# Performance work log

Hardware: AMD Instinct MI355X
Metric: run time of the kernel (lower is better)

## Reference

```python
import jax, jax.numpy as jnp
import numpy as np
import math

DENOM = 32.0

# e3nn scalar_activation normalizes the activation to unit second moment under N(0,1).
# Compute the gelu normalization constant by Gauss-Hermite quadrature.
_zs, _ws = np.polynomial.hermite_e.hermegauss(64)
_g = 0.5 * _zs * (1.0 + np.array([math.erf(z / math.sqrt(2.0)) for z in _zs]))
C_GELU = float(1.0 / math.sqrt((_ws * _g * _g).sum() / math.sqrt(2.0 * math.pi)))


def _spherical_harmonics(r):
    # r: [E,3] unit vectors. Component-normalized real SH for l=1,2,3.
    x, y, z = r[..., 0], r[..., 1], r[..., 2]
    s3, s5, s15 = math.sqrt(3.0), math.sqrt(5.0), math.sqrt(15.0)
    s7, s105 = math.sqrt(7.0), math.sqrt(105.0)
    s35_8, s21_8 = math.sqrt(35.0 / 8.0), math.sqrt(21.0 / 8.0)
    Y1 = s3 * r                                                     # [E,3]
    Y2 = jnp.stack([s15 * x * y, s15 * y * z, 0.5 * s5 * (3 * z * z - 1),
                    s15 * x * z, 0.5 * s15 * (x * x - y * y)], -1)   # [E,5]
    Y3 = jnp.stack([s35_8 * y * (3 * x * x - y * y), s105 * x * y * z,
                    s21_8 * y * (5 * z * z - 1), 0.5 * s7 * z * (5 * z * z - 3),
                    s21_8 * x * (5 * z * z - 1), 0.5 * s105 * z * (x * x - y * y),
                    s35_8 * x * (x * x - 3 * y * y)], -1)            # [E,7]
    return [Y1, Y2, Y3]


def setup_inputs() -> dict:
    key = jax.random.key(0)
    k = jax.random.split(key, 7)
    N, E, MUL, TMUL = 32768, 1048576, 16, 32
    return {
        "x": jax.random.normal(k[0], (N, MUL), jnp.float32),
        "positions": jax.random.normal(k[1], (N, 3), jnp.float32),
        "W_pre": jax.random.normal(k[2], (4, MUL, TMUL), jnp.float32),
        "W_post": jax.random.normal(k[3], (4, TMUL, TMUL), jnp.float32),
        "W_shortcut": jax.random.normal(k[4], (MUL, TMUL), jnp.float32),
        "senders": jax.random.randint(k[5], (E,), 0, N, jnp.int32),
        "receivers": jax.random.randint(k[6], (E,), 0, N, jnp.int32),
    }


def reference(x, positions, W_pre, W_post, W_shortcut, senders, receivers):
    N, mul = x.shape
    tmul = W_pre.shape[-1]
    # --- edge update: sh of relative positions, tensor product with sender scalars ---
    rvec = positions[receivers] - positions[senders]                 # [E,3]
    n = jnp.linalg.norm(rvec, axis=-1, keepdims=True)
    rhat = rvec / jnp.where(n == 0, 1.0, n)
    Ys = _spherical_harmonics(rhat)
    s = x[senders]                                                   # [E,mul] (0e)
    # --- aggregate edge features at receivers (segment sum) ---
    agg = [jax.ops.segment_sum(s, receivers, num_segments=N)]        # 0e block
    for Y in Ys:
        e = (s[:, :, None] * Y[:, None, :]).reshape(s.shape[0], -1)  # 0e x l -> l
        agg.append(jax.ops.segment_sum(e, receivers, num_segments=N).reshape(N, mul, Y.shape[-1]))
    # --- node update: linear_pre -> scalar act -> linear_post, plus shortcut ---
    inv_in = 1.0 / math.sqrt(mul)
    inv_mid = 1.0 / math.sqrt(tmul)
    out = []
    for l in range(4):
        a = agg[l] / DENOM
        if l == 0:
            p = (a @ W_pre[0]) * inv_in
            p = C_GELU * jax.nn.gelu(p, approximate=False)           # act on 0e scalars only
            q = (p @ W_post[0]) * inv_mid
            q = q + (x @ W_shortcut) * inv_in                        # shortcut: only 0e path exists
            out.append(q)
        else:
            p = jnp.einsum('nui,uv->nvi', a, W_pre[l]) * inv_in
            q = jnp.einsum('nvi,vw->nwi', p, W_post[l]) * inv_mid
            out.append(q.reshape(N, -1))
    return jnp.concatenate(out, axis=-1)                              # [N, tmul*16]
```

## Files before the change

kernel.cpp:

```cpp
#include <hip/hip_runtime.h>
#include <math.h>

#define NN 32768
#define EN 1048576
#define NBIN 256
#define BINCAP 8192
#define TILE 4096

#define C_GELU_F 1.5335262f

__global__ __launch_bounds__(512) void bin_k(const int* __restrict__ snd,
                                             const int* __restrict__ rcv,
                                             const float* __restrict__ pos,
                                             float4* __restrict__ posw,
                                             int* __restrict__ bin_cur,
                                             unsigned* __restrict__ binbuf) {
    __shared__ unsigned cnt[NBIN];
    __shared__ unsigned excl[NBIN];
    __shared__ unsigned cur2[NBIN];
    __shared__ unsigned gbase[NBIN];
    __shared__ unsigned stage[TILE];
    int t = threadIdx.x;
    int tile = blockIdx.x * TILE;
    if (t < NBIN) { cnt[t] = 0; cur2[t] = 0; }
    if (t < 128) {
        int n = (blockIdx.x << 7) + t;
        posw[n] = make_float4(pos[3*n], pos[3*n+1], pos[3*n+2], 0.f);
    }
    __syncthreads();

    unsigned w[TILE / 512];
#pragma unroll
    for (int i = 0; i < TILE / 512; ++i) {
        int e = tile + i * 512 + t;
        unsigned r = (unsigned)rcv[e], s = (unsigned)snd[e];
        w[i] = (r << 15) | s;
        atomicAdd(&cnt[w[i] >> 22], 1u);
    }
    __syncthreads();

    unsigned my = (t < NBIN) ? cnt[t] : 0u;
    if (t < NBIN) excl[t] = my;
    __syncthreads();
    for (int d = 1; d < NBIN; d <<= 1) {
        unsigned v = (t < NBIN && t >= d) ? excl[t - d] : 0u;
        __syncthreads();
        if (t < NBIN) excl[t] += v;
        __syncthreads();
    }
    if (t < NBIN) {
        unsigned myexcl = excl[t] - my;
        gbase[t] = atomicAdd((unsigned*)&bin_cur[t], my);
        excl[t] = myexcl;
    }
    __syncthreads();

#pragma unroll
    for (int i = 0; i < TILE / 512; ++i) {
        unsigned b = w[i] >> 22;
        unsigned p = excl[b] + atomicAdd(&cur2[b], 1u);
        stage[p] = w[i];
    }
    __syncthreads();

    for (int p = t; p < TILE; p += 512) {
        unsigned ww = stage[p];
        unsigned b = ww >> 22;
        unsigned idx = gbase[b] + ((unsigned)p - excl[b]);
        if (idx < BINCAP) binbuf[b * BINCAP + idx] = ww;
    }
}

__global__ __launch_bounds__(1024) void csr_k(const int* __restrict__ bin_cur,
                                              const unsigned* __restrict__ binbuf,
                                              int* __restrict__ row_ptr,
                                              int* __restrict__ edge_csr) {
    __shared__ unsigned sc[NBIN];
    __shared__ unsigned cnt[128];
    __shared__ unsigned excl[128];
    __shared__ unsigned cur2[128];
    int b = blockIdx.x;
    int t = threadIdx.x;

    if (t < NBIN) sc[t] = (unsigned)bin_cur[t];
    __syncthreads();
    for (int d = 1; d < NBIN; d <<= 1) {
        unsigned v = (t < NBIN && t >= d) ? sc[t - d] : 0u;
        __syncthreads();
        if (t < NBIN) sc[t] += v;
        __syncthreads();
    }
    int Mraw = bin_cur[b];
    int base = (int)(sc[b] - (unsigned)Mraw);
    int M = Mraw > BINCAP ? BINCAP : Mraw;
    if (t < 128) { cnt[t] = 0; cur2[t] = 0; }
    __syncthreads();

    const unsigned* bb = binbuf + b * BINCAP;
    for (int i = t; i < M; i += 1024)
        atomicAdd(&cnt[(bb[i] >> 15) & 127], 1u);
    __syncthreads();

    if (t < 128) excl[t] = cnt[t];
    __syncthreads();
    for (int d = 1; d < 128; d <<= 1) {
        unsigned v = (t >= d && t < 128) ? excl[t - d] : 0u;
        __syncthreads();
        if (t < 128) excl[t] += v;
        __syncthreads();
    }
    if (t < 128) {
        unsigned e = excl[t] - cnt[t];
        excl[t] = e;
        row_ptr[(b << 7) + t] = base + (int)e;
        if (b == NBIN - 1 && t == 127) row_ptr[NN] = base + (int)(e + cnt[127]);
    }
    __syncthreads();

    for (int i = t; i < M; i += 1024) {
        unsigned ww = bb[i];
        unsigned r7 = (ww >> 15) & 127;
        unsigned dst = excl[r7] + atomicAdd(&cur2[r7], 1u);
        edge_csr[base + dst] = (int)(ww & 0x7FFF);
    }
}

#define GROUPS 32
#define BLK 512
#define YST 20
#define GST (16*YST + 8)

__global__ __launch_bounds__(512, 4) void fused_k(const float* __restrict__ x,
                                                  const float4* __restrict__ posw,
                                                  const int* __restrict__ row_ptr,
                                                  const int* __restrict__ edge_csr,
                                                  const float* __restrict__ Wpre,
                                                  const float* __restrict__ Wpost,
                                                  const float* __restrict__ Wsc,
                                                  float* __restrict__ out) {
    __shared__ float sPre[4*516];
    __shared__ float sPost[4*1028];
    __shared__ float sSc[512];
    __shared__ float sY[GROUPS * GST];

    int t = threadIdx.x;
    for (int idx = t; idx < 2048; idx += BLK)
        sPre[(idx >> 9)*516 + (idx & 511)] = Wpre[idx];
    for (int idx = t; idx < 4096; idx += BLK)
        sPost[(idx >> 10)*1028 + (idx & 1023)] = Wpost[idx];
    sSc[t] = Wsc[t];
    __syncthreads();

    int g = t >> 4;
    int j = t & 15;
    int n = blockIdx.x * GROUPS + g;
    int beg = row_ptr[n], end = row_ptr[n + 1];
    int cnt = end - beg;
    float4 rp = posw[n];
    float* yg = sY + g * GST;

    const float s3   = 1.7320508075688772f;
    const float s5   = 2.2360679774997896f;
    const float s15  = 3.8729833462074170f;
    const float s7   = 2.6457513110645907f;
    const float s105 = 10.246950765959598f;
    const float s35_8 = 2.0916500663351889f;
    const float s21_8 = 1.6201851746019651f;

    float acc[16];
#pragma unroll
    for (int u = 0; u < 16; ++u) acc[u] = 0.f;

    int nch = (cnt + 15) >> 4;
    if (nch > 0) {
        int ki0 = (j < cnt) ? j : cnt - 1;
        int sE = edge_csr[beg + ki0];
        float4 sp = posw[sE];

        for (int c = 0; c < nch; ++c) {
            int kn = ((c + 1) << 4) + j;
            int kiN = (kn < cnt) ? kn : cnt - 1;
            int sEn = edge_csr[beg + kiN];

            float vx = rp.x - sp.x, vy = rp.y - sp.y, vz = rp.z - sp.z;
            float n2 = vx*vx + vy*vy + vz*vz;
            float inv;
            if (n2 > 0.f) {
                inv = rsqrtf(n2);
                inv = inv * (1.5f - 0.5f * n2 * inv * inv);
            } else inv = 0.f;
            float X = vx*inv, Y = vy*inv, Z = vz*inv;
            float XX = X*X, YY = Y*Y, ZZ = Z*Z;
            float m = (((c << 4) + j) < cnt) ? 1.f : 0.f;

            float* yr = yg + j * YST;
            ((float4*)yr)[0] = make_float4(m, m*(s3*X), m*(s3*Y), m*(s3*Z));
            ((float4*)yr)[1] = make_float4(m*(s15*X*Y), m*(s15*Y*Z),
                                           m*(0.5f*s5*(3.f*ZZ - 1.f)), m*(s15*X*Z));
            ((float4*)yr)[2] = make_float4(m*(0.5f*s15*(XX - YY)),
                                           m*(s35_8*Y*(3.f*XX - YY)),
                                           m*(s105*X*Y*Z),
                                           m*(s21_8*Y*(5.f*ZZ - 1.f)));
            ((float4*)yr)[3] = make_float4(m*(0.5f*s7*Z*(5.f*ZZ - 3.f)),
                                           m*(s21_8*X*(5.f*ZZ - 1.f)),
                                           m*(0.5f*s105*Z*(XX - YY)),
                                           m*(s35_8*X*(XX - 3.f*YY)));

            int se[16];
#pragma unroll
            for (int e = 0; e < 16; ++e)
                se[e] = __shfl(sE, (t & 48) + e, 64);
            float yt[16];
#pragma unroll
            for (int e = 0; e < 16; ++e)
                yt[e] = yg[e * YST + j];

            float4 spn = posw[sEn];

#pragma unroll
            for (int e = 0; e < 16; ++e) {
                float y = yt[e];
                const float4* xp = (const float4*)(x + (se[e] << 4));
                float4 a0 = xp[0], a1 = xp[1], a2 = xp[2], a3 = xp[3];
                acc[0]  += a0.x * y;  acc[1]  += a0.y * y;
                acc[2]  += a0.z * y;  acc[3]  += a0.w * y;
                acc[4]  += a1.x * y;  acc[5]  += a1.y * y;
                acc[6]  += a1.z * y;  acc[7]  += a1.w * y;
                acc[8]  += a2.x * y;  acc[9]  += a2.y * y;
                acc[10] += a2.z * y;  acc[11] += a2.w * y;
                acc[12] += a3.x * y;  acc[13] += a3.y * y;
                acc[14] += a3.z * y;  acc[15] += a3.w * y;
            }

            sE = sEn; sp = spn;
        }
    }

    int l, i, offl, deg;
    if (j == 0)      { l = 0; i = 0;     offl = 0;   deg = 1; }
    else if (j < 4)  { l = 1; i = j - 1; offl = 32;  deg = 3; }
    else if (j < 9)  { l = 2; i = j - 4; offl = 128; deg = 5; }
    else             { l = 3; i = j - 9; offl = 288; deg = 7; }

    const float c1 = 0.0078125f;
    const float c2 = 0.17677669529663687f;

    float p[32];
#pragma unroll
    for (int v = 0; v < 32; ++v) p[v] = 0.f;
    const float* wp = sPre + l * 516;
#pragma unroll
    for (int uu = 0; uu < 16; ++uu) {
        float a = acc[uu];
        const float4* w4 = (const float4*)(wp + (uu << 5));
#pragma unroll
        for (int vq = 0; vq < 8; ++vq) {
            float4 w = w4[vq];
            p[4*vq+0] += a * w.x;
            p[4*vq+1] += a * w.y;
            p[4*vq+2] += a * w.z;
            p[4*vq+3] += a * w.w;
        }
    }
#pragma unroll
    for (int v = 0; v < 32; ++v) p[v] *= c1;

    if (j == 0) {
#pragma unroll
        for (int v = 0; v < 32; ++v) {
            float pv = p[v];
            p[v] = C_GELU_F * 0.5f * pv * (1.f + erff(pv * 0.7071067811865476f));
        }
    }

    float q[32];
#pragma unroll
    for (int w = 0; w < 32; ++w) q[w] = 0.f;
    const float* wq = sPost + l * 1028;
#pragma unroll
    for (int v = 0; v < 32; ++v) {
        float pv = p[v];
        const float4* w4 = (const float4*)(wq + (v << 5));
#pragma unroll
        for (int wd = 0; wd < 8; ++wd) {
            float4 w = w4[wd];
            q[4*wd+0] += pv * w.x;
            q[4*wd+1] += pv * w.y;
            q[4*wd+2] += pv * w.z;
            q[4*wd+3] += pv * w.w;
        }
    }
#pragma unroll
    for (int w = 0; w < 32; ++w) q[w] *= c2;

    if (j == 0) {
        const float* xp = x + (n << 4);
#pragma unroll
        for (int uu = 0; uu < 16; ++uu) {
            float xv = 0.25f * xp[uu];
            const float4* w4 = (const float4*)(sSc + (uu << 5));
#pragma unroll
            for (int wd = 0; wd < 8; ++wd) {
                float4 w = w4[wd];
                q[4*wd+0] += xv * w.x;
                q[4*wd+1] += xv * w.y;
                q[4*wd+2] += xv * w.z;
                q[4*wd+3] += xv * w.w;
            }
        }
    }

    float* op = out + (n << 9) + offl + i;
#pragma unroll
    for (int w = 0; w < 32; ++w) op[w * deg] = q[w];
}

extern "C" void kernel_launch(void* const* d_in, const int* in_sizes, int n_in,
                              void* d_out, int out_size, void* d_ws, size_t ws_size,
                              hipStream_t stream) {
    const float* x     = (const float*)d_in[0];
    const float* pos   = (const float*)d_in[1];
    const float* Wpre  = (const float*)d_in[2];
    const float* Wpost = (const float*)d_in[3];
    const float* Wsc   = (const float*)d_in[4];
    const int*   snd   = (const int*)d_in[5];
    const int*   rcv   = (const int*)d_in[6];
    float* out = (float*)d_out;

    char* ws = (char*)d_ws;
    int*      bin_cur   = (int*)(ws);
    int*      row_ptr   = (int*)(ws + 2048);
    float4*   posw      = (float4*)(ws + 0x30000);
    int*      edge_csr  = (int*)(ws + 0xB0000);
    unsigned* binbuf    = (unsigned*)(ws + 0x500000);

    hipMemsetAsync(bin_cur, 0, NBIN * sizeof(int), stream);
    bin_k<<<EN / TILE, 512, 0, stream>>>(snd, rcv, pos, posw, bin_cur, binbuf);
    csr_k<<<NBIN, 1024, 0, stream>>>(bin_cur, binbuf, row_ptr, edge_csr);
    fused_k<<<NN / GROUPS, BLK, 0, stream>>>(x, posw, row_ptr, edge_csr,
                                             Wpre, Wpost, Wsc, out);
}
```

Before: 186.1 us.

## Fold per-bin CSR construction into the fused node kernel, dropping csr_k

Raises the bin count to 1024 so each bin holds exactly the 32 receiver nodes that one fused_k block handles. Each fused_k block now loads its bin from binbuf, counting-sorts the edges by receiver in shared memory (16-bit sender ids, wave-level scan), and uses the resulting offsets directly. This removes the separate csr_k launch and the global row_ptr/edge_csr round trip. In exchange, bin_k scatters each tile into four times as many bins with fewer entries per bin, which makes its global writes less coalesced, and every fused block pays for a shared-memory sort before its main loop.

```diff
diff --git a/kernel.cpp b/kernel.cpp
--- a/kernel.cpp
+++ b/kernel.cpp
@@ -3,9 +3,9 @@
 
 #define NN 32768
 #define EN 1048576
-#define NBIN 256
-#define BINCAP 8192
-#define TILE 4096
+#define NBIN 1024
+#define BINCAP 2048
+#define TILE 2048
 
 #define C_GELU_F 1.5335262f
 
@@ -22,9 +22,9 @@
     __shared__ unsigned stage[TILE];
     int t = threadIdx.x;
     int tile = blockIdx.x * TILE;
-    if (t < NBIN) { cnt[t] = 0; cur2[t] = 0; }
-    if (t < 128) {
-        int n = (blockIdx.x << 7) + t;
+    cnt[t] = 0; cnt[t + 512] = 0; cur2[t] = 0; cur2[t + 512] = 0;
+    if (t < 64) {
+        int n = (blockIdx.x << 6) + t;
         posw[n] = make_float4(pos[3*n], pos[3*n+1], pos[3*n+2], 0.f);
     }
     __syncthreads();
@@ -35,29 +35,28 @@
         int e = tile + i * 512 + t;
         unsigned r = (unsigned)rcv[e], s = (unsigned)snd[e];
         w[i] = (r << 15) | s;
-        atomicAdd(&cnt[w[i] >> 22], 1u);
-    }
-    __syncthreads();
-
-    unsigned my = (t < NBIN) ? cnt[t] : 0u;
-    if (t < NBIN) excl[t] = my;
+        atomicAdd(&cnt[w[i] >> 20], 1u);
+    }
+    __syncthreads();
+
+    unsigned my0 = cnt[t], my1 = cnt[t + 512];
+    excl[t] = my0; excl[t + 512] = my1;
     __syncthreads();
     for (int d = 1; d < NBIN; d <<= 1) {
-        unsigned v = (t < NBIN && t >= d) ? excl[t - d] : 0u;
+        unsigned v0 = (t >= d) ? excl[t - d] : 0u;
+        unsigned v1 = excl[t + 512 - d];
         __syncthreads();
-        if (t < NBIN) excl[t] += v;
+        excl[t] += v0; excl[t + 512] += v1;
         __syncthreads();
     }
-    if (t < NBIN) {
-        unsigned myexcl = excl[t] - my;
-        gbase[t] = atomicAdd((unsigned*)&bin_cur[t], my);
-        excl[t] = myexcl;
-    }
+    gbase[t]       = atomicAdd((unsigned*)&bin_cur[t], my0);
+    gbase[t + 512] = atomicAdd((unsigned*)&bin_cur[t + 512], my1);
+    excl[t] -= my0; excl[t + 512] -= my1;
     __syncthreads();
 
 #pragma unroll
     for (int i = 0; i < TILE / 512; ++i) {
-        unsigned b = w[i] >> 22;
+        unsigned b = w[i] >> 20;
         unsigned p = excl[b] + atomicAdd(&cur2[b], 1u);
         stage[p] = w[i];
     }
@@ -65,63 +64,9 @@
 
     for (int p = t; p < TILE; p += 512) {
         unsigned ww = stage[p];
-        unsigned b = ww >> 22;
+        unsigned b = ww >> 20;
         unsigned idx = gbase[b] + ((unsigned)p - excl[b]);
         if (idx < BINCAP) binbuf[b * BINCAP + idx] = ww;
-    }
-}
-
-__global__ __launch_bounds__(1024) void csr_k(const int* __restrict__ bin_cur,
-                                              const unsigned* __restrict__ binbuf,
-                                              int* __restrict__ row_ptr,
-                                              int* __restrict__ edge_csr) {
-    __shared__ unsigned sc[NBIN];
-    __shared__ unsigned cnt[128];
-    __shared__ unsigned excl[128];
-    __shared__ unsigned cur2[128];
-    int b = blockIdx.x;
-    int t = threadIdx.x;
-
-    if (t < NBIN) sc[t] = (unsigned)bin_cur[t];
-    __syncthreads();
-    for (int d = 1; d < NBIN; d <<= 1) {
-        unsigned v = (t < NBIN && t >= d) ? sc[t - d] : 0u;
-        __syncthreads();
-        if (t < NBIN) sc[t] += v;
-        __syncthreads();
-    }
-    int Mraw = bin_cur[b];
-    int base = (int)(sc[b] - (unsigned)Mraw);
-    int M = Mraw > BINCAP ? BINCAP : Mraw;
-    if (t < 128) { cnt[t] = 0; cur2[t] = 0; }
-    __syncthreads();
-
-    const unsigned* bb = binbuf + b * BINCAP;
-    for (int i = t; i < M; i += 1024)
-        atomicAdd(&cnt[(bb[i] >> 15) & 127], 1u);
-    __syncthreads();
-
-    if (t < 128) excl[t] = cnt[t];
-    __syncthreads();
-    for (int d = 1; d < 128; d <<= 1) {
-        unsigned v = (t >= d && t < 128) ? excl[t - d] : 0u;
-        __syncthreads();
-        if (t < 128) excl[t] += v;
-        __syncthreads();
-    }
-    if (t < 128) {
-        unsigned e = excl[t] - cnt[t];
-        excl[t] = e;
-        row_ptr[(b << 7) + t] = base + (int)e;
-        if (b == NBIN - 1 && t == 127) row_ptr[NN] = base + (int)(e + cnt[127]);
-    }
-    __syncthreads();
-
-    for (int i = t; i < M; i += 1024) {
-        unsigned ww = bb[i];
-        unsigned r7 = (ww >> 15) & 127;
-        unsigned dst = excl[r7] + atomicAdd(&cur2[r7], 1u);
-        edge_csr[base + dst] = (int)(ww & 0x7FFF);
     }
 }
 
@@ -132,8 +77,8 @@
 
 __global__ __launch_bounds__(512, 4) void fused_k(const float* __restrict__ x,
                                                   const float4* __restrict__ posw,
-                                                  const int* __restrict__ row_ptr,
-                                                  const int* __restrict__ edge_csr,
+                                                  const int* __restrict__ bin_cur,
+                                                  const unsigned* __restrict__ binbuf,
                                                   const float* __restrict__ Wpre,
                                                   const float* __restrict__ Wpost,
                                                   const float* __restrict__ Wsc,
@@ -142,20 +87,55 @@
     __shared__ float sPost[4*1028];
     __shared__ float sSc[512];
     __shared__ float sY[GROUPS * GST];
+    __shared__ unsigned short sEdge[BINCAP];
+    __shared__ unsigned sCnt[32];
+    __shared__ unsigned sExcl[32];
+    __shared__ unsigned sCur[32];
 
     int t = threadIdx.x;
+    int b = blockIdx.x;
+
     for (int idx = t; idx < 2048; idx += BLK)
         sPre[(idx >> 9)*516 + (idx & 511)] = Wpre[idx];
     for (int idx = t; idx < 4096; idx += BLK)
         sPost[(idx >> 10)*1028 + (idx & 1023)] = Wpost[idx];
     sSc[t] = Wsc[t];
+    if (t < 32) { sCnt[t] = 0; sCur[t] = 0; }
+
+    int M = bin_cur[b]; M = M > BINCAP ? BINCAP : M;
+    unsigned* sRaw = (unsigned*)sY;
+    __syncthreads();
+
+    for (int i = t; i < M; i += BLK) {
+        unsigned ww = binbuf[b * BINCAP + i];
+        sRaw[i] = ww;
+        atomicAdd(&sCnt[(ww >> 15) & 31], 1u);
+    }
+    __syncthreads();
+    if (t < 32) {
+        unsigned val = sCnt[t];
+        unsigned inc = val;
+#pragma unroll
+        for (int d = 1; d < 32; d <<= 1) {
+            unsigned v = __shfl_up(inc, d, 32);
+            if (t >= d) inc += v;
+        }
+        sExcl[t] = inc - val;
+    }
+    __syncthreads();
+    for (int i = t; i < M; i += BLK) {
+        unsigned ww = sRaw[i];
+        unsigned r5 = (ww >> 15) & 31;
+        unsigned dst = sExcl[r5] + atomicAdd(&sCur[r5], 1u);
+        sEdge[dst] = (unsigned short)(ww & 0x7FFF);
+    }
     __syncthreads();
 
     int g = t >> 4;
     int j = t & 15;
-    int n = blockIdx.x * GROUPS + g;
-    int beg = row_ptr[n], end = row_ptr[n + 1];
-    int cnt = end - beg;
+    int n = (b << 5) + g;
+    int beg = (int)sExcl[g];
+    int cnt = (int)sCnt[g];
     float4 rp = posw[n];
     float* yg = sY + g * GST;
 
@@ -174,13 +154,13 @@
     int nch = (cnt + 15) >> 4;
     if (nch > 0) {
         int ki0 = (j < cnt) ? j : cnt - 1;
-        int sE = edge_csr[beg + ki0];
+        int sE = (int)sEdge[beg + ki0];
         float4 sp = posw[sE];
 
         for (int c = 0; c < nch; ++c) {
             int kn = ((c + 1) << 4) + j;
             int kiN = (kn < cnt) ? kn : cnt - 1;
-            int sEn = edge_csr[beg + kiN];
+            int sEn = (int)sEdge[beg + kiN];
 
             float vx = rp.x - sp.x, vy = rp.y - sp.y, vz = rp.z - sp.z;
             float n2 = vx*vx + vy*vy + vz*vz;
@@ -329,14 +309,11 @@
 
     char* ws = (char*)d_ws;
     int*      bin_cur   = (int*)(ws);
-    int*      row_ptr   = (int*)(ws + 2048);
     float4*   posw      = (float4*)(ws + 0x30000);
-    int*      edge_csr  = (int*)(ws + 0xB0000);
     unsigned* binbuf    = (unsigned*)(ws + 0x500000);
 
     hipMemsetAsync(bin_cur, 0, NBIN * sizeof(int), stream);
     bin_k<<<EN / TILE, 512, 0, stream>>>(snd, rcv, pos, posw, bin_cur, binbuf);
-    csr_k<<<NBIN, 1024, 0, stream>>>(bin_cur, binbuf, row_ptr, edge_csr);
-    fused_k<<<NN / GROUPS, BLK, 0, stream>>>(x, posw, row_ptr, edge_csr,
-                                             Wpre, Wpost, Wsc, out);
+    fused_k<<<NBIN, BLK, 0, stream>>>(x, posw, bin_cur, binbuf,
+                                      Wpre, Wpost, Wsc, out);
 }
```

Result: slower. 191.7 us (+3.0%).
